# Performance work log

Measured on AMD Instinct MI355X. Metric: run time of the kernel, lower is better.

The kernel has to match this reference:

```python
import jax, jax.numpy as jnp
import numpy as np

H, N, L = 1024, 64, 2          # d_model, d_state, n_layers
B, T, STEPS = 32, 512, 16


def setup_inputs():
    key = jax.random.key(0)
    ks = jax.random.split(key, 12)
    inp = {}
    inp["input_seq"] = jax.random.normal(ks[0], (B, T, 1), jnp.float32)
    inp["autoregressive_steps"] = STEPS
    # input_proj: Linear(1, d_model)
    inp["in_proj_w"] = jax.random.normal(ks[1], (1, H), jnp.float32)
    inp["in_proj_b"] = jnp.zeros((H,), jnp.float32)
    # per-layer diagonal S4 (S4D-style) params, stacked over layers
    inp["log_dt"] = jnp.log(1e-3) + jax.random.uniform(ks[2], (L, H), jnp.float32) * (jnp.log(1e-1) - jnp.log(1e-3))
    inp["A_re"] = -0.5 * jnp.ones((L, H, N), jnp.float32)
    inp["A_im"] = jnp.broadcast_to(jnp.pi * jnp.arange(N, dtype=jnp.float32), (L, H, N)) + jnp.zeros((L, H, N), jnp.float32)
    inp["B_re"] = jax.random.normal(ks[3], (L, H, N), jnp.float32)
    inp["B_im"] = jax.random.normal(ks[4], (L, H, N), jnp.float32)
    inp["C_re"] = jax.random.normal(ks[5], (L, H, N), jnp.float32) / np.sqrt(N)
    inp["C_im"] = jax.random.normal(ks[6], (L, H, N), jnp.float32) / np.sqrt(N)
    inp["D"] = jax.random.normal(ks[7], (L, H), jnp.float32)
    # S4Block output linear with GLU: Linear(H, 2H) then glu
    inp["out_w"] = jax.random.normal(ks[8], (L, H, 2 * H), jnp.float32) / np.sqrt(H)
    inp["out_b"] = jnp.zeros((L, 2 * H), jnp.float32)
    inp["ln_g"] = jnp.ones((L, H), jnp.float32)
    inp["ln_b"] = jnp.zeros((L, H), jnp.float32)
    # output_layer: Linear(d_model, 1)
    inp["head_w"] = jax.random.normal(ks[9], (H, 1), jnp.float32) / np.sqrt(H)
    inp["head_b"] = jnp.zeros((1,), jnp.float32)
    return inp


def _ln(x, g, b, eps=1e-5):
    m = x.mean(-1, keepdims=True)
    v = jnp.var(x, axis=-1, keepdims=True)
    return (x - m) / jnp.sqrt(v + eps) * g + b


def _glu(z):
    a, b = jnp.split(z, 2, axis=-1)
    return a * jax.nn.sigmoid(b)


def _forward(input_seq, in_proj_w, in_proj_b, log_dt, A_re, A_im, B_re, B_im,
             C_re, C_im, D, out_w, out_b, ln_g, ln_b, head_w, head_b, steps):
    Bb = input_seq.shape[0]
    A = A_re + 1j * A_im                              # (L,H,N) complex64
    dt = jnp.exp(log_dt)[..., None]                   # (L,H,1)
    dA = jnp.exp(dt * A)                              # ZOH discretization
    dB = (dA - 1.0) / A * (B_re + 1j * B_im)
    C = C_re + 1j * C_im

    def s4_seq(u, j):  # u: (B,T,H) -> (B,T,H), recurrence over the full sequence
        s0 = jnp.zeros((Bb, H, N), dA.dtype)
        def step(s, ut):  # ut: (B,H)
            s = dA[j] * s + dB[j] * ut[..., None]
            y = 2.0 * jnp.einsum('hn,bhn->bh', C[j], s).real + D[j] * ut
            return s, y
        _, ys = jax.lax.scan(step, s0, jnp.swapaxes(u, 0, 1))
        return jnp.swapaxes(ys, 0, 1)

    # ---- encoder pass over the input sequence ----
    x = input_seq @ in_proj_w + in_proj_b             # (B,T,H)
    for j in range(L):
        res = x
        y = s4_seq(x, j)
        y = jax.nn.gelu(y, approximate=False)
        y = _glu(y @ out_w[j] + out_b[j])
        x = _ln(y + res, ln_g[j], ln_b[j])
    context = x[:, -1, :]                             # (B,H)

    def dec_step(carry, i):
        dec_in, states = carry                        # (B,), (L,B,H,N) complex
        u0 = jnp.broadcast_to(dec_in[:, None], (Bb, H))   # scalar broadcast to d_model
        dec = u0
        new_states = []
        for j in range(L):
            s = dA[j] * states[j] + dB[j] * dec[..., None]
            y = 2.0 * jnp.einsum('hn,bhn->bh', C[j], s).real + D[j] * dec
            y = jax.nn.gelu(y, approximate=False)
            y = _glu(y @ out_w[j] + out_b[j])
            res = jnp.where(i == 0, u0, y)            # step 0: raw-input residual; else self-residual
            dec = _ln(y + res, ln_g[j], ln_b[j])
            new_states.append(s)
        dec = dec + context
        bit = jax.nn.sigmoid(dec @ head_w + head_b)   # (B,1)
        return (bit[:, 0], jnp.stack(new_states)), bit

    s_init = jnp.zeros((L, Bb, H, N), dA.dtype)
    d_init = jnp.zeros((Bb,), input_seq.dtype)
    _, outs = jax.lax.scan(dec_step, (d_init, s_init), jnp.arange(steps))
    return jnp.swapaxes(outs, 0, 1)                   # (B, steps, 1)


def reference(input_seq, in_proj_w, in_proj_b, log_dt, A_re, A_im, B_re, B_im,
              C_re, C_im, D, out_w, out_b, ln_g, ln_b, head_w, head_b,
              autoregressive_steps):
    return _forward(input_seq, in_proj_w, in_proj_b, log_dt, A_re, A_im, B_re,
                    B_im, C_re, C_im, D, out_w, out_b, ln_g, ln_b, head_w,
                    head_b, autoregressive_steps)
```

## Files before the change

kernel.cpp:

```cpp
#include <hip/hip_runtime.h>
#include <hip/hip_bf16.h>
#include <math.h>

#define H    1024
#define NST  64
#define LAYN 2
#define BSZ  32
#define TLEN 512
#define NSTEPS 16
#define H2   2048
#define FLAGSTRIDE 32
#define NGRP 8

typedef __attribute__((ext_vector_type(8))) short bf16x8;
typedef __attribute__((ext_vector_type(4))) float f32x4;

__device__ __forceinline__ float gelu_f(float x){
    return 0.5f*x*(1.0f+erff(x*0.7071067811865475f));
}
__device__ __forceinline__ float sigm_f(float x){
    return 1.0f/(1.0f+expf(-x));
}
__device__ __forceinline__ short bfbits(float x){
    __hip_bfloat16 h = __float2bfloat16(x);
    return *(short*)&h;
}
__device__ __forceinline__ float bf2f(short s){
    unsigned int u = ((unsigned int)(unsigned short)s) << 16;
    return __uint_as_float(u);
}
__device__ __forceinline__ void gload16(const void* g, void* l){
    __builtin_amdgcn_global_load_lds((const __attribute__((address_space(1))) void*)g,
                                     (__attribute__((address_space(3))) void*)l, 16, 0, 0);
}
__device__ __forceinline__ void ast(float* p, float v){
    __hip_atomic_store(p, v, __ATOMIC_RELAXED, __HIP_MEMORY_SCOPE_AGENT);
}
__device__ __forceinline__ float ald(const float* p){
    return __hip_atomic_load(p, __ATOMIC_RELAXED, __HIP_MEMORY_SCOPE_AGENT);
}

__global__ void k_precompute(const float* __restrict__ log_dt,
                             const float* __restrict__ Are, const float* __restrict__ Aim,
                             const float* __restrict__ Bre, const float* __restrict__ Bim,
                             float* __restrict__ dAr, float* __restrict__ dAi,
                             float* __restrict__ dBr, float* __restrict__ dBi){
    int i = blockIdx.x*256 + threadIdx.x;
    if (i >= LAYN*H*NST) return;
    int lh = i / NST;
    float dt = expf(log_dt[lh]);
    float ar = Are[i], ai = Aim[i];
    float e  = expf(dt*ar);
    float sa, ca; sincosf(dt*ai, &sa, &ca);
    float dar = e*ca, dai = e*sa;
    float zr = dar-1.0f, zi = dai;
    float inv = 1.0f/(ar*ar + ai*ai);
    float wr = (zr*ar + zi*ai)*inv;
    float wi = (zi*ar - zr*ai)*inv;
    float br = Bre[i], bi = Bim[i];
    dAr[i]=dar; dAi[i]=dai;
    dBr[i]=wr*br - wi*bi;
    dBi[i]=wr*bi + wi*br;
}

__global__ void k_inproj_x(const float* __restrict__ in, const float* __restrict__ w,
                           const float* __restrict__ bias, float* __restrict__ x){
    int i = blockIdx.x*256+threadIdx.x;
    int h = i & (H-1);
    int bt = i >> 10;
    x[i] = in[bt]*w[h] + bias[h];
}
__global__ void k_inproj_xT(const float* __restrict__ in, const float* __restrict__ w,
                            const float* __restrict__ bias, float* __restrict__ xT){
    int i = blockIdx.x*256+threadIdx.x;
    int t = i & (TLEN-1);
    int bh = i >> 9;
    int h = bh & (H-1);
    int b = bh >> 10;
    xT[i] = in[b*TLEN + t]*w[h] + bias[h];
}

__global__ __launch_bounds__(64) void k_genK(
        const float* __restrict__ dAr, const float* __restrict__ dAi,
        const float* __restrict__ dBr, const float* __restrict__ dBi,
        const float* __restrict__ Cre, const float* __restrict__ Cim,
        float* __restrict__ Kbuf){
    __shared__ float trans[16][65];
    int lh = blockIdx.x;
    int lane = threadIdx.x;
    int pi = lh*NST + lane;
    float ar=dAr[pi], ai=dAi[pi];
    float br=dBr[pi], bi=dBi[pi];
    float cr=2.f*Cre[pi], ci=2.f*Cim[pi];
    float wr = cr*br - ci*bi;
    float wi = cr*bi + ci*br;
    float* Krow = Kbuf + (size_t)lh*TLEN;
    int r = lane>>2, q = lane&3;
    for (int c=0;c<TLEN/16;c++){
        #pragma unroll
        for (int i=0;i<16;i++){
            trans[i][lane] = wr;
            float nr = fmaf(wr,ar, -wi*ai);
            float ni = fmaf(wr,ai,  wi*ar);
            wr=nr; wi=ni;
        }
        __syncthreads();
        float s = 0.f;
        #pragma unroll
        for (int m=0;m<16;m++) s += trans[r][q*16+m];
        s += __shfl_xor(s,1,64);
        s += __shfl_xor(s,2,64);
        if (q==0) Krow[c*16 + r] = s;
        __syncthreads();
    }
}

#define CTT 256
#define CJT 64
__global__ __launch_bounds__(256) void k_conv(
        const float* __restrict__ u,
        const float* __restrict__ Kbuf,
        const float* __restrict__ Dv,
        __hip_bfloat16* __restrict__ g,
        int layer){
    __shared__ float u_s[CJT][33];
    __shared__ float Ks[CTT+CJT];
    int h  = blockIdx.y;
    int t0 = blockIdx.x * CTT;
    int tid = threadIdx.x;
    int bg = tid & 7;
    int tg = tid >> 3;
    const float* Krow = Kbuf + ((size_t)layer*H + h)*TLEN;
    float acc[8][4];
    #pragma unroll
    for (int i=0;i<8;i++){
        #pragma unroll
        for (int b=0;b<4;b++) acc[i][b]=0.f;
    }
    int ntile = t0/CJT + CTT/CJT;
    for (int jt=0; jt<ntile; jt++){
        int j0 = jt*CJT;
        __syncthreads();
        for (int i=tid; i<CTT+CJT; i+=256){
            int d = t0 - j0 - (CJT-1) + i;
            Ks[i] = (d>=0) ? Krow[d] : 0.f;
        }
        {
            int jj = tid & 63, bq = tid >> 6;
            #pragma unroll
            for (int p=0;p<8;p++){
                int b = bq + p*4;
                u_s[jj][b] = u[((size_t)b*H + h)*TLEN + j0 + jj];
            }
        }
        __syncthreads();
        #pragma unroll 8
        for (int j=0;j<CJT;j++){
            float4 ub = *(const float4*)&u_s[j][bg*4];
            int base = tg*8 + (CJT-1) - j;
            float kv[8];
            #pragma unroll
            for (int i=0;i<8;i++) kv[i] = Ks[base+i];
            #pragma unroll
            for (int i=0;i<8;i++){
                acc[i][0] = fmaf(kv[i], ub.x, acc[i][0]);
                acc[i][1] = fmaf(kv[i], ub.y, acc[i][1]);
                acc[i][2] = fmaf(kv[i], ub.z, acc[i][2]);
                acc[i][3] = fmaf(kv[i], ub.w, acc[i][3]);
            }
        }
    }
    float dv = Dv[layer*H + h];
    int tb = t0 + tg*8;
    #pragma unroll
    for (int b=0;b<4;b++){
        int bb = bg*4 + b;
        const float* urow = u + ((size_t)bb*H + h)*TLEN + tb;
        float4 u0 = *(const float4*)urow;
        float4 u1 = *(const float4*)(urow+4);
        bf16x8 o;
        o[0] = bfbits(gelu_f(fmaf(dv,u0.x, acc[0][b])));
        o[1] = bfbits(gelu_f(fmaf(dv,u0.y, acc[1][b])));
        o[2] = bfbits(gelu_f(fmaf(dv,u0.z, acc[2][b])));
        o[3] = bfbits(gelu_f(fmaf(dv,u0.w, acc[3][b])));
        o[4] = bfbits(gelu_f(fmaf(dv,u1.x, acc[4][b])));
        o[5] = bfbits(gelu_f(fmaf(dv,u1.y, acc[5][b])));
        o[6] = bfbits(gelu_f(fmaf(dv,u1.z, acc[6][b])));
        o[7] = bfbits(gelu_f(fmaf(dv,u1.w, acc[7][b])));
        *(bf16x8*)(g + ((size_t)bb*H + h)*TLEN + tb) = o;
    }
}

__global__ __launch_bounds__(256) void k_trcast_bf(const __hip_bfloat16* __restrict__ x,
                                                   __hip_bfloat16* __restrict__ y){
    __shared__ __hip_bfloat16 tile[32][34];
    int t0 = blockIdx.x*32, h0 = blockIdx.y*32, b = blockIdx.z;
    int tx = threadIdx.x & 31, ty = threadIdx.x >> 5;
    #pragma unroll
    for (int i=0;i<32;i+=8)
        tile[ty+i][tx] = x[((size_t)(b*H + h0+ty+i))*TLEN + t0+tx];
    __syncthreads();
    #pragma unroll
    for (int i=0;i<32;i+=8)
        y[((size_t)(b*TLEN + t0+ty+i))*H + h0+tx] = tile[tx][ty+i];
}

__global__ __launch_bounds__(256) void k_transpose(const float* __restrict__ x, float* __restrict__ xT){
    __shared__ float tile[32][33];
    int t0 = blockIdx.x*32, h0 = blockIdx.y*32, b = blockIdx.z;
    int tx = threadIdx.x & 31, ty = threadIdx.x >> 5;
    #pragma unroll
    for (int i=0;i<32;i+=8)
        tile[ty+i][tx] = x[((size_t)(b*TLEN + t0+ty+i))*H + h0+tx];
    __syncthreads();
    #pragma unroll
    for (int i=0;i<32;i+=8)
        xT[((size_t)(b*H + h0+ty+i))*TLEN + t0+tx] = tile[tx][ty+i];
}

__global__ __launch_bounds__(256) void k_wtr(const float* __restrict__ W,
                                             __hip_bfloat16* __restrict__ Wt){
    __shared__ float tile[32][33];
    int n0 = blockIdx.x*32, k0 = blockIdx.y*32, l = blockIdx.z;
    const float* Wl = W + (size_t)l*H*H2;
    __hip_bfloat16* Wtl = Wt + (size_t)l*H*H2;
    int tx = threadIdx.x & 31, ty = threadIdx.x >> 5;
    #pragma unroll
    for (int i=0;i<32;i+=8)
        tile[ty+i][tx] = Wl[(size_t)(k0+ty+i)*H2 + n0+tx];
    __syncthreads();
    #pragma unroll
    for (int i=0;i<32;i+=8)
        Wtl[(size_t)(n0+ty+i)*H + k0+tx] = __float2bfloat16(tile[tx][ty+i]);
}

__global__ __launch_bounds__(256) void k_gemm_glu_mfma(
        const __hip_bfloat16* __restrict__ Abf,
        const __hip_bfloat16* __restrict__ Wt,
        const float* __restrict__ bias2,
        float* __restrict__ glu){
    __shared__ alignas(16) short As[128*32];
    __shared__ alignas(16) short Bs[128*32];
    const int K = 1024;
    int tid = threadIdx.x;
    int lane = tid & 63, wid = tid >> 6;
    int m0 = blockIdx.x * 128;
    int nb = blockIdx.y * 64;
    int g0 = tid, g1 = tid + 256;
    int r0 = g0 >> 2, r1 = g1 >> 2;
    int wtr0 = nb + ((r0>>6)<<5) + (r0&31) + ((r0>>5)&1)*1024;
    int wtr1 = nb + ((r1>>6)<<5) + (r1&31) + ((r1>>5)&1)*1024;
    const short* Ap = (const short*)Abf;
    const short* Bp = (const short*)Wt;
    const short* Ag0 = Ap + (size_t)(m0 + r0)*K + (g0&3)*8;
    const short* Ag1 = Ap + (size_t)(m0 + r1)*K + (g1&3)*8;
    const short* Bg0 = Bp + (size_t)wtr0*K + (g0&3)*8;
    const short* Bg1 = Bp + (size_t)wtr1*K + (g1&3)*8;
    char* AsB = (char*)As;
    char* BsB = (char*)Bs;
    int wr = wid >> 1, wc = wid & 1;
    int mo = wr*64, no = wc*64;
    f32x4 acc[4][4] = {};
    int arow = (lane & 15)*32 + (lane>>4)*8;
    for (int k0 = 0; k0 < K; k0 += 32){
        gload16(Ag0 + k0, AsB + wid*1024);
        gload16(Ag1 + k0, AsB + 4096 + wid*1024);
        gload16(Bg0 + k0, BsB + wid*1024);
        gload16(Bg1 + k0, BsB + 4096 + wid*1024);
        asm volatile("s_waitcnt vmcnt(0)" ::: "memory");
        __syncthreads();
        bf16x8 a[4], b[4];
        #pragma unroll
        for (int mi=0;mi<4;mi++)
            a[mi] = *(const bf16x8*)(As + (mo + mi*16)*32 + arow);
        #pragma unroll
        for (int ni=0;ni<4;ni++)
            b[ni] = *(const bf16x8*)(Bs + (no + ni*16)*32 + arow);
        #pragma unroll
        for (int mi=0;mi<4;mi++){
            #pragma unroll
            for (int ni=0;ni<4;ni++){
                acc[mi][ni] = __builtin_amdgcn_mfma_f32_16x16x32_bf16(a[mi], b[ni], acc[mi][ni], 0, 0, 0);
            }
        }
        __syncthreads();
    }
    int cbase = nb + wc*32 + (lane&15);
    #pragma unroll
    for (int ni=0;ni<2;ni++){
        int c = cbase + ni*16;
        float ba = bias2[c], bb = bias2[c+1024];
        #pragma unroll
        for (int mi=0;mi<4;mi++){
            #pragma unroll
            for (int r=0;r<4;r++){
                size_t m = m0 + mo + mi*16 + (lane>>4)*4 + r;
                float za = acc[mi][ni][r] + ba;
                float zb = acc[mi][ni+2][r] + bb;
                glu[m*H + c] = za * sigm_f(zb);
            }
        }
    }
}

__global__ __launch_bounds__(256) void k_ln(const float* __restrict__ glu, const float* __restrict__ res,
        const float* __restrict__ gamma, const float* __restrict__ beta, float* __restrict__ outx){
    __shared__ float red[8];
    int row = blockIdx.x;
    int tid = threadIdx.x;
    float4 gv = *(const float4*)(glu + (size_t)row*H + tid*4);
    float4 rv = *(const float4*)(res + (size_t)row*H + tid*4);
    float x0=gv.x+rv.x, x1=gv.y+rv.y, x2=gv.z+rv.z, x3=gv.w+rv.w;
    float s = x0+x1+x2+x3;
    float q = x0*x0+x1*x1+x2*x2+x3*x3;
    #pragma unroll
    for (int m=32;m>=1;m>>=1){ s += __shfl_xor(s,m,64); q += __shfl_xor(q,m,64); }
    int wv = tid>>6;
    if ((tid&63)==0){ red[wv]=s; red[4+wv]=q; }
    __syncthreads();
    s = red[0]+red[1]+red[2]+red[3];
    q = red[4]+red[5]+red[6]+red[7];
    float m = s*(1.0f/H);
    float v = q*(1.0f/H) - m*m;
    float rstd = rsqrtf(v + 1e-5f);
    float4 gm = *(const float4*)(gamma + tid*4);
    float4 bt = *(const float4*)(beta + tid*4);
    float4 o;
    o.x = (x0-m)*rstd*gm.x + bt.x;
    o.y = (x1-m)*rstd*gm.y + bt.y;
    o.z = (x2-m)*rstd*gm.z + bt.z;
    o.w = (x3-m)*rstd*gm.w + bt.w;
    *(float4*)(outx + (size_t)row*H + tid*4) = o;
}

__global__ void k_ctx(const float* __restrict__ x, float* __restrict__ ctx){
    int i = blockIdx.x*256+threadIdx.x;
    int b = i>>10, h = i&(H-1);
    ctx[i] = x[((size_t)(b*TLEN + TLEN-1))*H + h];
}

__device__ __forceinline__ void gbar_grp(int* gfl, int jj, int g, int tid){
    __syncthreads();
    if (tid == 0)
        __hip_atomic_store(gfl + jj*FLAGSTRIDE, g, __ATOMIC_RELAXED,
                           __HIP_MEMORY_SCOPE_AGENT);
    if (tid < 32){
        int it = 0;
        while (__hip_atomic_load(gfl + tid*FLAGSTRIDE, __ATOMIC_RELAXED,
                                 __HIP_MEMORY_SCOPE_AGENT) < g){
            __builtin_amdgcn_s_sleep(1);
            if (++it > 1000000) break;
        }
    }
    __syncthreads();
}

__device__ __forceinline__ void gemv4(int grp, int jj, int tid,
        float (*ysh)[H], float (*part)[32][8],
        const short* __restrict__ Wl, const float* __restrict__ b2,
        const float* __restrict__ ygel, float* __restrict__ glud){
    #pragma unroll
    for (int i=0;i<16;i++){
        int idx = i*256 + tid;
        int b4 = idx >> 10, hh = idx & 1023;
        ysh[b4][hh] = ald(&ygel[(size_t)(4*grp + b4)*H + hh]);
    }
    __syncthreads();
    int p = tid & 31, ks = tid >> 5;
    int colp = jj*32 + p;
    const short* wza = Wl + (size_t)colp*H + ks*128;
    const short* wzb = Wl + (size_t)(colp+1024)*H + ks*128;
    float a0=0,a1=0,a2=0,a3=0, c0=0,c1=0,c2=0,c3=0;
    const float* u0 = &ysh[0][ks*128];
    const float* u1 = &ysh[1][ks*128];
    const float* u2 = &ysh[2][ks*128];
    const float* u3 = &ysh[3][ks*128];
    for (int kk=0; kk<128; kk+=8){
        bf16x8 wa = *(const bf16x8*)(wza + kk);
        bf16x8 wb = *(const bf16x8*)(wzb + kk);
        #pragma unroll
        for (int j=0;j<8;j++){
            float wav = bf2f(wa[j]), wbv = bf2f(wb[j]);
            float y0 = u0[kk+j], y1 = u1[kk+j], y2 = u2[kk+j], y3 = u3[kk+j];
            a0 = fmaf(y0, wav, a0);  c0 = fmaf(y0, wbv, c0);
            a1 = fmaf(y1, wav, a1);  c1 = fmaf(y1, wbv, c1);
            a2 = fmaf(y2, wav, a2);  c2 = fmaf(y2, wbv, c2);
            a3 = fmaf(y3, wav, a3);  c3 = fmaf(y3, wbv, c3);
        }
    }
    __syncthreads();
    part[ks][p][0]=a0; part[ks][p][1]=c0;
    part[ks][p][2]=a1; part[ks][p][3]=c1;
    part[ks][p][4]=a2; part[ks][p][5]=c2;
    part[ks][p][6]=a3; part[ks][p][7]=c3;
    __syncthreads();
    if (tid < 128){
        int p2 = tid & 31, b4 = tid >> 5;
        int c2 = jj*32 + p2;
        float sa=0.f, sb=0.f;
        #pragma unroll
        for (int q=0;q<8;q++){ sa += part[q][p2][b4*2]; sb += part[q][p2][b4*2+1]; }
        float za = sa + b2[c2];
        float zb = sb + b2[1024 + c2];
        ast(&glud[(size_t)(4*grp + b4)*H + c2], za * sigm_f(zb));
    }
}

__global__ __launch_bounds__(256, 1) void k_decode(
        const float* __restrict__ Kbuf, const float* __restrict__ Dv,
        const __hip_bfloat16* __restrict__ Wt, const float* __restrict__ bias2,
        const float* __restrict__ lng, const float* __restrict__ lnb,
        const float* __restrict__ ctx, const float* __restrict__ headw,
        const float* __restrict__ headb,
        float* __restrict__ ygel0, float* __restrict__ ygel1,
        float* __restrict__ glud0, float* __restrict__ glud1,
        float* __restrict__ out, int* __restrict__ flags){
    __shared__ float hist[16][H];
    __shared__ float ysh[4][H];
    __shared__ float part[8][32][8];
    __shared__ float red[8];
    __shared__ float bitsh[16];
    int bid = blockIdx.x;
    int grp = bid & 7, jj = bid >> 3;
    int tid = threadIdx.x;
    int lane = tid & 63, wv = tid >> 6;
    bool leader = (jj < 4);
    int b = grp*4 + jj;
    float4 dv0v, dv1v, lg0v, be0v, lg1v, be1v, cvxv, hwv;
    float hb = headb[0];
    if (leader){
        dv0v = *(const float4*)(Dv + tid*4);
        dv1v = *(const float4*)(Dv + H + tid*4);
        lg0v = *(const float4*)(lng + tid*4);
        be0v = *(const float4*)(lnb + tid*4);
        lg1v = *(const float4*)(lng + H + tid*4);
        be1v = *(const float4*)(lnb + H + tid*4);
        cvxv = *(const float4*)(ctx + (size_t)b*H + tid*4);
        hwv  = *(const float4*)(headw + tid*4);
    }
    if (tid < 16) bitsh[tid] = 0.f;
    __syncthreads();
    const short* Wt0 = (const short*)Wt;
    const short* Wt1 = (const short*)Wt + (size_t)H*H2;
    int* gfl = flags + grp*32*FLAGSTRIDE;
    int g = 1;
    for (int s=0; s<NSTEPS; s++){
        if (leader){
            if (s > 0){
                int sp = s-1;
                float x0 = ald(&glud1[(size_t)b*H + tid*4+0]);
                float x1 = ald(&glud1[(size_t)b*H + tid*4+1]);
                float x2 = ald(&glud1[(size_t)b*H + tid*4+2]);
                float x3 = ald(&glud1[(size_t)b*H + tid*4+3]);
                if (sp != 0){ x0*=2.f; x1*=2.f; x2*=2.f; x3*=2.f; }
                float su = x0+x1+x2+x3, qu = x0*x0+x1*x1+x2*x2+x3*x3;
                #pragma unroll
                for (int m=32;m>=1;m>>=1){ su += __shfl_xor(su,m,64); qu += __shfl_xor(qu,m,64); }
                if (lane==0){ red[wv]=su; red[4+wv]=qu; }
                __syncthreads();
                float S = red[0]+red[1]+red[2]+red[3];
                float Q = red[4]+red[5]+red[6]+red[7];
                float mean = S*(1.f/H), var = Q*(1.f/H)-mean*mean;
                float rstd = rsqrtf(var + 1e-5f);
                float d0 = (x0-mean)*rstd*lg1v.x + be1v.x + cvxv.x;
                float d1 = (x1-mean)*rstd*lg1v.y + be1v.y + cvxv.y;
                float d2 = (x2-mean)*rstd*lg1v.z + be1v.z + cvxv.z;
                float d3 = (x3-mean)*rstd*lg1v.w + be1v.w + cvxv.w;
                float hp = d0*hwv.x + d1*hwv.y + d2*hwv.z + d3*hwv.w;
                #pragma unroll
                for (int m=32;m>=1;m>>=1) hp += __shfl_xor(hp,m,64);
                __syncthreads();
                if (lane==0) red[wv] = hp;
                __syncthreads();
                float hs = red[0]+red[1]+red[2]+red[3] + hb;
                float bit = sigm_f(hs);
                if (tid==0){ out[b*NSTEPS + sp] = bit; bitsh[sp] = bit; }
                __syncthreads();
            }
            float bu = (s==0) ? 0.f : bitsh[s-1];
            float dvs[4] = {dv0v.x, dv0v.y, dv0v.z, dv0v.w};
            #pragma unroll
            for (int i=0;i<4;i++){
                int h = tid*4+i;
                const float* Kr = Kbuf + (size_t)h*TLEN;
                float y0 = dvs[i]*bu;
                #pragma unroll
                for (int d=0; d<16; d++){
                    int idx = s-1-d;
                    float uv = (idx >= 0) ? bitsh[idx] : 0.f;
                    y0 = fmaf(Kr[d], uv, y0);
                }
                ast(&ygel0[(size_t)b*H + h], gelu_f(y0));
            }
        }
        gbar_grp(gfl, jj, g++, tid);
        gemv4(grp, jj, tid, ysh, part, Wt0, bias2, ygel0, glud0);
        gbar_grp(gfl, jj, g++, tid);
        if (leader){
            float x0 = ald(&glud0[(size_t)b*H + tid*4+0]);
            float x1 = ald(&glud0[(size_t)b*H + tid*4+1]);
            float x2 = ald(&glud0[(size_t)b*H + tid*4+2]);
            float x3 = ald(&glud0[(size_t)b*H + tid*4+3]);
            if (s != 0){ x0*=2.f; x1*=2.f; x2*=2.f; x3*=2.f; }
            float su = x0+x1+x2+x3, qu = x0*x0+x1*x1+x2*x2+x3*x3;
            #pragma unroll
            for (int m=32;m>=1;m>>=1){ su += __shfl_xor(su,m,64); qu += __shfl_xor(qu,m,64); }
            if (lane==0){ red[wv]=su; red[4+wv]=qu; }
            __syncthreads();
            float S = red[0]+red[1]+red[2]+red[3];
            float Q = red[4]+red[5]+red[6]+red[7];
            float mean = S*(1.f/H), var = Q*(1.f/H)-mean*mean;
            float rstd = rsqrtf(var + 1e-5f);
            float dd[4];
            dd[0] = (x0-mean)*rstd*lg0v.x + be0v.x;
            dd[1] = (x1-mean)*rstd*lg0v.y + be0v.y;
            dd[2] = (x2-mean)*rstd*lg0v.z + be0v.z;
            dd[3] = (x3-mean)*rstd*lg0v.w + be0v.w;
            float dvs[4] = {dv1v.x, dv1v.y, dv1v.z, dv1v.w};
            #pragma unroll
            for (int i=0;i<4;i++){
                int h = tid*4+i;
                hist[s & 15][h] = dd[i];
                const float* Kr = Kbuf + (size_t)(H+h)*TLEN;
                float y1 = dvs[i]*dd[i];
                #pragma unroll
                for (int d=0; d<16; d++){
                    int sd = s-d;
                    float uv = (sd >= 0) ? hist[sd & 15][h] : 0.f;
                    y1 = fmaf(Kr[d], uv, y1);
                }
                ast(&ygel1[(size_t)b*H + h], gelu_f(y1));
            }
        }
        gbar_grp(gfl, jj, g++, tid);
        gemv4(grp, jj, tid, ysh, part, Wt1, bias2 + H2, ygel1, glud1);
        gbar_grp(gfl, jj, g++, tid);
    }
    if (leader){
        float x0 = 2.f*ald(&glud1[(size_t)b*H + tid*4+0]);
        float x1 = 2.f*ald(&glud1[(size_t)b*H + tid*4+1]);
        float x2 = 2.f*ald(&glud1[(size_t)b*H + tid*4+2]);
        float x3 = 2.f*ald(&glud1[(size_t)b*H + tid*4+3]);
        float su = x0+x1+x2+x3, qu = x0*x0+x1*x1+x2*x2+x3*x3;
        #pragma unroll
        for (int m=32;m>=1;m>>=1){ su += __shfl_xor(su,m,64); qu += __shfl_xor(qu,m,64); }
        if (lane==0){ red[wv]=su; red[4+wv]=qu; }
        __syncthreads();
        float S = red[0]+red[1]+red[2]+red[3];
        float Q = red[4]+red[5]+red[6]+red[7];
        float mean = S*(1.f/H), var = Q*(1.f/H)-mean*mean;
        float rstd = rsqrtf(var + 1e-5f);
        float d0 = (x0-mean)*rstd*lg1v.x + be1v.x + cvxv.x;
        float d1 = (x1-mean)*rstd*lg1v.y + be1v.y + cvxv.y;
        float d2 = (x2-mean)*rstd*lg1v.z + be1v.z + cvxv.z;
        float d3 = (x3-mean)*rstd*lg1v.w + be1v.w + cvxv.w;
        float hp = d0*hwv.x + d1*hwv.y + d2*hwv.z + d3*hwv.w;
        #pragma unroll
        for (int m=32;m>=1;m>>=1) hp += __shfl_xor(hp,m,64);
        __syncthreads();
        if (lane==0) red[wv] = hp;
        __syncthreads();
        float hs = red[0]+red[1]+red[2]+red[3] + hb;
        if (tid==0) out[b*NSTEPS + 15] = sigm_f(hs);
    }
}

extern "C" void kernel_launch(void* const* d_in, const int* in_sizes, int n_in,
                              void* d_out, int out_size, void* d_ws, size_t ws_size,
                              hipStream_t stream) {
    const float* in_seq = (const float*)d_in[0];
    const float* inw  = (const float*)d_in[2];
    const float* inb  = (const float*)d_in[3];
    const float* log_dt = (const float*)d_in[4];
    const float* Are = (const float*)d_in[5];
    const float* Aim = (const float*)d_in[6];
    const float* Bre = (const float*)d_in[7];
    const float* Bim = (const float*)d_in[8];
    const float* Cre = (const float*)d_in[9];
    const float* Cim = (const float*)d_in[10];
    const float* Dv  = (const float*)d_in[11];
    const float* outw = (const float*)d_in[12];
    const float* outb = (const float*)d_in[13];
    const float* lng = (const float*)d_in[14];
    const float* lnb = (const float*)d_in[15];
    const float* headw = (const float*)d_in[16];
    const float* headb = (const float*)d_in[17];
    float* out = (float*)d_out;

    float* ws = (float*)d_ws;
    size_t off = 0;
    auto alloc = [&](size_t n){ float* p = ws + off; off += n; return p; };
    float* dAr = alloc((size_t)LAYN*H*NST);
    float* dAi = alloc((size_t)LAYN*H*NST);
    float* dBr = alloc((size_t)LAYN*H*NST);
    float* dBi = alloc((size_t)LAYN*H*NST);
    float* Kbuf = alloc((size_t)LAYN*H*TLEN);
    float* bufA = alloc((size_t)BSZ*TLEN*H);
    float* bufB = alloc((size_t)BSZ*TLEN*H);
    __hip_bfloat16* gbf = (__hip_bfloat16*)alloc((size_t)BSZ*TLEN*H/2);
    __hip_bfloat16* Abf = (__hip_bfloat16*)alloc((size_t)BSZ*TLEN*H/2);
    __hip_bfloat16* Wt  = (__hip_bfloat16*)alloc((size_t)LAYN*H*H2/2);
    float* ctx = alloc((size_t)BSZ*H);
    float* ygel0 = alloc((size_t)BSZ*H);
    float* ygel1 = alloc((size_t)BSZ*H);
    float* glud0 = alloc((size_t)BSZ*H);
    float* glud1 = alloc((size_t)BSZ*H);
    int*   flags = (int*)alloc((size_t)NGRP*32*FLAGSTRIDE);

    k_precompute<<<(LAYN*H*NST+255)/256, 256, 0, stream>>>(log_dt,Are,Aim,Bre,Bim,dAr,dAi,dBr,dBi);
    k_genK<<<LAYN*H, 64, 0, stream>>>(dAr,dAi,dBr,dBi,Cre,Cim,Kbuf);
    k_wtr<<<dim3(H2/32, H/32, LAYN), 256, 0, stream>>>(outw, Wt);
    k_inproj_x <<<(BSZ*TLEN*H)/256, 256, 0, stream>>>(in_seq, inw, inb, bufA);
    k_inproj_xT<<<(BSZ*TLEN*H)/256, 256, 0, stream>>>(in_seq, inw, inb, bufB);

    k_conv<<<dim3(TLEN/CTT, H), 256, 0, stream>>>(bufB, Kbuf, Dv, gbf, 0);
    k_trcast_bf<<<dim3(TLEN/32, H/32, BSZ), 256, 0, stream>>>(gbf, Abf);
    k_gemm_glu_mfma<<<dim3(BSZ*TLEN/128, H/64), 256, 0, stream>>>(Abf, Wt, outb, bufB);
    k_ln<<<BSZ*TLEN, 256, 0, stream>>>(bufB, bufA, lng, lnb, bufA);
    k_transpose<<<dim3(16,32,32), 256, 0, stream>>>(bufA, bufB);

    k_conv<<<dim3(TLEN/CTT, H), 256, 0, stream>>>(bufB, Kbuf, Dv, gbf, 1);
    k_trcast_bf<<<dim3(TLEN/32, H/32, BSZ), 256, 0, stream>>>(gbf, Abf);
    k_gemm_glu_mfma<<<dim3(BSZ*TLEN/128, H/64), 256, 0, stream>>>(Abf, Wt + (size_t)H*H2, outb + H2, bufB);
    k_ln<<<BSZ*TLEN, 256, 0, stream>>>(bufB, bufA, lng+H, lnb+H, bufA);

    k_ctx<<<(BSZ*H)/256, 256, 0, stream>>>(bufA, ctx);

    hipMemsetAsync(flags, 0, sizeof(int)*(size_t)NGRP*32*FLAGSTRIDE, stream);
    k_decode<<<NGRP*32, 256, 0, stream>>>(Kbuf, Dv, Wt, outb, lng, lnb,
                                          ctx, headw, headb,
                                          ygel0, ygel1, glud0, glud1, out, flags);
}
```

Before: 1.489 ms.

## Compute causal convolution as Toeplitz bf16 MFMA matmul per channel

Replaces the scalar FP32 FMA causal convolution with a per-channel Toeplitz matrix product on bf16 MFMA instructions. The kernel stages the reversed kernel as bf16 in shared memory, using 8 shifted copies so any offset gives an aligned 8-element load. The whole sequence for all 32 batches also goes to shared memory in bf16. Upper-triangular tiles are skipped. This moves the dominant conv arithmetic onto matrix cores, at the cost of bf16 rounding of the inputs and kernel, and a grid of only 1024 blocks.

```diff
diff --git a/kernel.cpp b/kernel.cpp
--- a/kernel.cpp
+++ b/kernel.cpp
@@ -115,79 +115,66 @@
     }
 }
 
-#define CTT 256
-#define CJT 64
-__global__ __launch_bounds__(256) void k_conv(
+__global__ __launch_bounds__(256, 2) void k_conv_mfma(
         const float* __restrict__ u,
         const float* __restrict__ Kbuf,
         const float* __restrict__ Dv,
         __hip_bfloat16* __restrict__ g,
         int layer){
-    __shared__ float u_s[CJT][33];
-    __shared__ float Ks[CTT+CJT];
-    int h  = blockIdx.y;
-    int t0 = blockIdx.x * CTT;
+    __shared__ short Krp[8][1040];
+    __shared__ short u_s[32][520];
+    int h = blockIdx.x;
     int tid = threadIdx.x;
-    int bg = tid & 7;
-    int tg = tid >> 3;
     const float* Krow = Kbuf + ((size_t)layer*H + h)*TLEN;
-    float acc[8][4];
-    #pragma unroll
-    for (int i=0;i<8;i++){
-        #pragma unroll
-        for (int b=0;b<4;b++) acc[i][b]=0.f;
-    }
-    int ntile = t0/CJT + CTT/CJT;
-    for (int jt=0; jt<ntile; jt++){
-        int j0 = jt*CJT;
-        __syncthreads();
-        for (int i=tid; i<CTT+CJT; i+=256){
-            int d = t0 - j0 - (CJT-1) + i;
-            Ks[i] = (d>=0) ? Krow[d] : 0.f;
-        }
-        {
-            int jj = tid & 63, bq = tid >> 6;
-            #pragma unroll
-            for (int p=0;p<8;p++){
-                int b = bq + p*4;
-                u_s[jj][b] = u[((size_t)b*H + h)*TLEN + j0 + jj];
-            }
-        }
-        __syncthreads();
-        #pragma unroll 8
-        for (int j=0;j<CJT;j++){
-            float4 ub = *(const float4*)&u_s[j][bg*4];
-            int base = tg*8 + (CJT-1) - j;
-            float kv[8];
-            #pragma unroll
-            for (int i=0;i<8;i++) kv[i] = Ks[base+i];
-            #pragma unroll
-            for (int i=0;i<8;i++){
-                acc[i][0] = fmaf(kv[i], ub.x, acc[i][0]);
-                acc[i][1] = fmaf(kv[i], ub.y, acc[i][1]);
-                acc[i][2] = fmaf(kv[i], ub.z, acc[i][2]);
-                acc[i][3] = fmaf(kv[i], ub.w, acc[i][3]);
-            }
+    for (int idx = tid; idx < 8*1040; idx += 256){
+        int c = idx / 1040, y = idx - c*1040;
+        int x = y + c;
+        float v = (x <= 511) ? Krow[511 - x] : 0.f;
+        Krp[c][y] = bfbits(v);
+    }
+    for (int idx = tid; idx < 32*512; idx += 256){
+        int b = idx >> 9, t = idx & 511;
+        u_s[b][t] = bfbits(u[((size_t)b*H + h)*TLEN + t]);
+    }
+    __syncthreads();
+    int w = tid >> 6, lane = tid & 63;
+    int m = lane & 15, q = lane >> 4;
+    f32x4 acc[8][2] = {};
+    for (int jt = 0; jt < 16; ++jt){
+        int jtile = jt*32;
+        bf16x8 b0 = *(const bf16x8*)&u_s[m][jtile + q*8];
+        bf16x8 b1 = *(const bf16x8*)&u_s[16 + m][jtile + q*8];
+        int mi_min = (2*jt - w + 3) >> 2;
+        if (mi_min < 0) mi_min = 0;
+        #pragma unroll
+        for (int mi = 0; mi < 8; ++mi){
+            if (mi < mi_min) continue;
+            int tb = (mi*4 + w)*16 + m;
+            int x0 = 511 - tb + jtile + q*8;
+            int c = x0 & 7, base = x0 - c;
+            bf16x8 a = *(const bf16x8*)&Krp[c][base];
+            acc[mi][0] = __builtin_amdgcn_mfma_f32_16x16x32_bf16(a, b0, acc[mi][0], 0,0,0);
+            acc[mi][1] = __builtin_amdgcn_mfma_f32_16x16x32_bf16(a, b1, acc[mi][1], 0,0,0);
         }
     }
     float dv = Dv[layer*H + h];
-    int tb = t0 + tg*8;
-    #pragma unroll
-    for (int b=0;b<4;b++){
-        int bb = bg*4 + b;
-        const float* urow = u + ((size_t)bb*H + h)*TLEN + tb;
-        float4 u0 = *(const float4*)urow;
-        float4 u1 = *(const float4*)(urow+4);
-        bf16x8 o;
-        o[0] = bfbits(gelu_f(fmaf(dv,u0.x, acc[0][b])));
-        o[1] = bfbits(gelu_f(fmaf(dv,u0.y, acc[1][b])));
-        o[2] = bfbits(gelu_f(fmaf(dv,u0.z, acc[2][b])));
-        o[3] = bfbits(gelu_f(fmaf(dv,u0.w, acc[3][b])));
-        o[4] = bfbits(gelu_f(fmaf(dv,u1.x, acc[4][b])));
-        o[5] = bfbits(gelu_f(fmaf(dv,u1.y, acc[5][b])));
-        o[6] = bfbits(gelu_f(fmaf(dv,u1.z, acc[6][b])));
-        o[7] = bfbits(gelu_f(fmaf(dv,u1.w, acc[7][b])));
-        *(bf16x8*)(g + ((size_t)bb*H + h)*TLEN + tb) = o;
+    #pragma unroll
+    for (int mi = 0; mi < 8; ++mi){
+        int tb2 = (mi*4 + w)*16 + (lane>>4)*4;
+        #pragma unroll
+        for (int nf = 0; nf < 2; ++nf){
+            int b = nf*16 + (lane & 15);
+            short4 o;
+            float uu0 = bf2f(u_s[b][tb2+0]);
+            float uu1 = bf2f(u_s[b][tb2+1]);
+            float uu2 = bf2f(u_s[b][tb2+2]);
+            float uu3 = bf2f(u_s[b][tb2+3]);
+            o.x = bfbits(gelu_f(fmaf(dv, uu0, acc[mi][nf][0])));
+            o.y = bfbits(gelu_f(fmaf(dv, uu1, acc[mi][nf][1])));
+            o.z = bfbits(gelu_f(fmaf(dv, uu2, acc[mi][nf][2])));
+            o.w = bfbits(gelu_f(fmaf(dv, uu3, acc[mi][nf][3])));
+            *(short4*)((short*)g + ((size_t)b*H + h)*TLEN + tb2) = o;
+        }
     }
 }
 
@@ -613,13 +600,13 @@
     k_inproj_x <<<(BSZ*TLEN*H)/256, 256, 0, stream>>>(in_seq, inw, inb, bufA);
     k_inproj_xT<<<(BSZ*TLEN*H)/256, 256, 0, stream>>>(in_seq, inw, inb, bufB);
 
-    k_conv<<<dim3(TLEN/CTT, H), 256, 0, stream>>>(bufB, Kbuf, Dv, gbf, 0);
+    k_conv_mfma<<<dim3(H), 256, 0, stream>>>(bufB, Kbuf, Dv, gbf, 0);
     k_trcast_bf<<<dim3(TLEN/32, H/32, BSZ), 256, 0, stream>>>(gbf, Abf);
     k_gemm_glu_mfma<<<dim3(BSZ*TLEN/128, H/64), 256, 0, stream>>>(Abf, Wt, outb, bufB);
     k_ln<<<BSZ*TLEN, 256, 0, stream>>>(bufB, bufA, lng, lnb, bufA);
     k_transpose<<<dim3(16,32,32), 256, 0, stream>>>(bufA, bufB);
 
-    k_conv<<<dim3(TLEN/CTT, H), 256, 0, stream>>>(bufB, Kbuf, Dv, gbf, 1);
+    k_conv_mfma<<<dim3(H), 256, 0, stream>>>(bufB, Kbuf, Dv, gbf, 1);
     k_trcast_bf<<<dim3(TLEN/32, H/32, BSZ), 256, 0, stream>>>(gbf, Abf);
     k_gemm_glu_mfma<<<dim3(BSZ*TLEN/128, H/64), 256, 0, stream>>>(Abf, Wt + (size_t)H*H2, outb + H2, bufB);
     k_ln<<<BSZ*TLEN, 256, 0, stream>>>(bufB, bufA, lng+H, lnb+H, bufA);
```

After: 1.237 ms. 1.2x faster.
